# Kernel optimization log

Hardware: AMD Instinct MI355X
Metric: run time of the kernel (lower is better)

The kernel has to match this reference:

```python
import jax, jax.numpy as jnp
import numpy as np

H = 12          # num attention heads
D_HEAD = 64     # head size (768 / 12)
P = 2           # power-law exponent
C = 5.0         # score shift
EPS = 1e-10


def setup_inputs() -> dict:
    key = jax.random.key(0)
    ks = jax.random.split(key, 8)
    B, S, Dm = 32, 512, 768
    scale = 1.0 / np.sqrt(Dm)
    return {
        "hidden_states": jax.random.normal(ks[0], (B, S, Dm), dtype=jnp.float32),
        "attention_mask": jnp.ones((B, 1, 1, S), dtype=jnp.float32),
        "Wq": jax.random.normal(ks[1], (Dm, Dm), dtype=jnp.float32) * scale,
        "bq": jnp.zeros((Dm,), dtype=jnp.float32),
        "Wk": jax.random.normal(ks[2], (Dm, Dm), dtype=jnp.float32) * scale,
        "bk": jnp.zeros((Dm,), dtype=jnp.float32),
        "Wv": jax.random.normal(ks[3], (Dm, Dm), dtype=jnp.float32) * scale,
        "bv": jnp.zeros((Dm,), dtype=jnp.float32),
    }


def _heads(x, B, S):
    # [B, S, H*d] -> [B, H, S, d]
    return x.reshape(B, S, H, D_HEAD).transpose(0, 2, 1, 3)


def reference(hidden_states, attention_mask, Wq, bq, Wk, bk, Wv, bv):
    B, S, Dm = hidden_states.shape
    q = _heads(hidden_states @ Wq + bq, B, S)
    k = _heads(hidden_states @ Wk + bk, B, S)
    v = _heads(hidden_states @ Wv + bv, B, S)

    inv_sqrt_d = 1.0 / (np.sqrt(D_HEAD) + 1e-10)
    scores = jnp.einsum("bhqd,bhkd->bhqk", q, k) * inv_sqrt_d  # [B,H,S,S]

    # Power-law attention (Powerformer, distill=0 branch)
    probs = jnp.power(scores + C, P)
    probs = probs / (jnp.sum(probs, axis=-1, keepdims=True) + EPS)
    probs = probs * attention_mask  # mask multiplied after normalization

    ctx = jnp.einsum("bhqk,bhkd->bhqd", probs, v)  # [B,H,S,d]
    ctx = ctx.transpose(0, 2, 1, 3).reshape(B, S, Dm)
    return ctx
```

## Files before the change

### kernel.cpp

```cpp
#include <hip/hip_runtime.h>

typedef __attribute__((ext_vector_type(8))) _Float16 half8;
typedef __attribute__((ext_vector_type(4))) _Float16 half4;
typedef __attribute__((ext_vector_type(4))) float f32x4;

#define MFMA16(a, b, c) __builtin_amdgcn_mfma_f32_16x16x32_f16((a), (b), (c), 0, 0, 0)


__global__ __launch_bounds__(256) void wcast_kernel(
    const float* __restrict__ W0, const float* __restrict__ W1,
    const float* __restrict__ W2,
    _Float16* __restrict__ T0, _Float16* __restrict__ T1,
    _Float16* __restrict__ T2)
{
    int z = blockIdx.z;
    const float* W = (z == 0) ? W0 : (z == 1) ? W1 : W2;
    _Float16* T = (z == 0) ? T0 : (z == 1) ? T1 : T2;
    __shared__ float tile[32][33];
    int n0 = blockIdx.x * 32, k0 = blockIdx.y * 32;
    int tx = threadIdx.x & 31, ty = threadIdx.x >> 5;
#pragma unroll
    for (int r = 0; r < 4; ++r)
        tile[ty + 8 * r][tx] = W[(size_t)(k0 + ty + 8 * r) * 768 + n0 + tx];
    __syncthreads();
#pragma unroll
    for (int r = 0; r < 4; ++r)
        T[(size_t)(n0 + ty + 8 * r) * 768 + k0 + tx] =
            (_Float16)tile[tx][ty + 8 * r];
}

__global__ __launch_bounds__(256) void qkv_gemm(
    const float* __restrict__ X,
    const _Float16* __restrict__ W0, const _Float16* __restrict__ W1,
    const _Float16* __restrict__ W2,
    const float* __restrict__ b0, const float* __restrict__ b1,
    const float* __restrict__ b2,
    _Float16* __restrict__ Qo, _Float16* __restrict__ Ko,
    _Float16* __restrict__ Vo)
{
    int z = blockIdx.z;
    const _Float16* Wt = (z == 0) ? W0 : (z == 1) ? W1 : W2;
    const float* bias = (z == 0) ? b0 : (z == 1) ? b1 : b2;
    _Float16* outp = (z == 0) ? Qo : (z == 1) ? Ko : Vo;

    int m0 = blockIdx.x * 128;
    int n0 = blockIdx.y * 128;

    __shared__ _Float16 As[128 * 40];
    __shared__ _Float16 Bs[128 * 40];

    int t = threadIdx.x;
    int wave = t >> 6, lane = t & 63, quad = lane >> 4, l16 = lane & 15;
    int wm = (wave & 1) * 64, wn = (wave >> 1) * 64;
    int arow = t >> 1, ahalf = t & 1;

    f32x4 acc[4][4] = {};

    for (int k0 = 0; k0 < 768; k0 += 32) {
        {
            const float* xp = X + (size_t)(m0 + arow) * 768 + k0 + ahalf * 16;
            float4 x0 = ((const float4*)xp)[0];
            float4 x1 = ((const float4*)xp)[1];
            float4 x2 = ((const float4*)xp)[2];
            float4 x3 = ((const float4*)xp)[3];
            half8 h0, h1;
            h0[0] = (_Float16)x0.x; h0[1] = (_Float16)x0.y;
            h0[2] = (_Float16)x0.z; h0[3] = (_Float16)x0.w;
            h0[4] = (_Float16)x1.x; h0[5] = (_Float16)x1.y;
            h0[6] = (_Float16)x1.z; h0[7] = (_Float16)x1.w;
            h1[0] = (_Float16)x2.x; h1[1] = (_Float16)x2.y;
            h1[2] = (_Float16)x2.z; h1[3] = (_Float16)x2.w;
            h1[4] = (_Float16)x3.x; h1[5] = (_Float16)x3.y;
            h1[6] = (_Float16)x3.z; h1[7] = (_Float16)x3.w;
            *(half8*)&As[arow * 40 + ahalf * 16] = h0;
            *(half8*)&As[arow * 40 + ahalf * 16 + 8] = h1;
        }
        {
            const _Float16* wp = Wt + (size_t)(n0 + arow) * 768 + k0 + ahalf * 16;
            half8 w0v = ((const half8*)wp)[0];
            half8 w1v = ((const half8*)wp)[1];
            *(half8*)&Bs[arow * 40 + ahalf * 16] = w0v;
            *(half8*)&Bs[arow * 40 + ahalf * 16 + 8] = w1v;
        }
        __syncthreads();

        half8 af[4], bfr[4];
#pragma unroll
        for (int i = 0; i < 4; ++i)
            af[i] = *(const half8*)&As[(wm + i * 16 + l16) * 40 + quad * 8];
#pragma unroll
        for (int j = 0; j < 4; ++j)
            bfr[j] = *(const half8*)&Bs[(wn + j * 16 + l16) * 40 + quad * 8];
#pragma unroll
        for (int i = 0; i < 4; ++i)
#pragma unroll
            for (int j = 0; j < 4; ++j)
                acc[i][j] = MFMA16(af[i], bfr[j], acc[i][j]);
        __syncthreads();
    }

#pragma unroll
    for (int j = 0; j < 4; ++j) {
        int n = n0 + wn + j * 16 + l16;
        float bv = bias[n];
        int hh = n >> 6, d = n & 63;
#pragma unroll
        for (int i = 0; i < 4; ++i) {
            int mbase = m0 + wm + i * 16 + quad * 4;
            if (z < 2) {
#pragma unroll
                for (int r = 0; r < 4; ++r) {
                    int m = mbase + r;
                    int bb = m >> 9, s = m & 511;
                    size_t off = (((size_t)(bb * 12 + hh)) * 512 + s) * 64 + d;
                    outp[off] = (_Float16)(acc[i][j][r] + bv);
                }
            } else {
                int bb = mbase >> 9, s = mbase & 511;
                half4 pk;
#pragma unroll
                for (int r = 0; r < 4; ++r)
                    pk[r] = (_Float16)(acc[i][j][r] + bv);
                size_t off = (((size_t)(bb * 12 + hh)) * 64 + d) * 512 + s;
                *(half4*)&outp[off] = pk;
            }
        }
    }
}

__global__ __launch_bounds__(256) void attn_kernel(
    const _Float16* __restrict__ Q, const _Float16* __restrict__ K,
    const _Float16* __restrict__ Vt, const float* __restrict__ mask,
    float* __restrict__ out)
{
    __shared__ _Float16 Ks[64 * 72];
    __shared__ _Float16 Vs[64 * 72];
    __shared__ _Float16 Ps[4][32 * 72];
    __shared__ float Ms[64];

    int t = threadIdx.x;
    int wave = t >> 6, lane = t & 63, quad = lane >> 4, l16 = lane & 15;
    int qt = blockIdx.x, h = blockIdx.y, b = blockIdx.z;
    size_t bh = (size_t)b * 12 + h;
    const _Float16* Qp = Q + bh * (512 * 64);
    const _Float16* Kp = K + bh * (512 * 64);
    const _Float16* Vp = Vt + bh * (64 * 512);
    int qbase = qt * 128 + wave * 32;

    half8 qf[2][2];
#pragma unroll
    for (int i = 0; i < 2; ++i)
#pragma unroll
        for (int ks = 0; ks < 2; ++ks)
            qf[i][ks] = *(const half8*)(Qp + (size_t)(qbase + i * 16 + l16) * 64 +
                                        ks * 32 + quad * 8);

    f32x4 ctx[2][4] = {};
    float rs[2][4] = {};

    int skey = t >> 2, spart = t & 3;

    for (int kt = 0; kt < 8; ++kt) {
        int k0 = kt * 64;
        __syncthreads();
        {
            const half8* kg = (const half8*)(Kp + (size_t)(k0 + skey) * 64 + spart * 16);
            half8 a0 = kg[0], a1 = kg[1];
            *(half8*)&Ks[skey * 72 + spart * 16] = a0;
            *(half8*)&Ks[skey * 72 + spart * 16 + 8] = a1;
            const half8* vg = (const half8*)(Vp + (size_t)skey * 512 + k0 + spart * 16);
            half8 v0 = vg[0], v1 = vg[1];
            *(half8*)&Vs[skey * 72 + spart * 16] = v0;
            *(half8*)&Vs[skey * 72 + spart * 16 + 8] = v1;
            if (t < 64) Ms[t] = mask[(size_t)b * 512 + k0 + t];
        }
        __syncthreads();

#pragma unroll
        for (int i = 0; i < 2; ++i) {
#pragma unroll
            for (int n = 0; n < 4; ++n) {
                f32x4 sc = {0.f, 0.f, 0.f, 0.f};
#pragma unroll
                for (int ks = 0; ks < 2; ++ks) {
                    half8 kf = *(const half8*)&Ks[(n * 16 + l16) * 72 + ks * 32 + quad * 8];
                    sc = MFMA16(qf[i][ks], kf, sc);
                }
                float mk = Ms[n * 16 + l16];
#pragma unroll
                for (int r = 0; r < 4; ++r) {
                    float s = sc[r] * 0.125f + 5.0f;
                    float w = s * s;
                    rs[i][r] += w;
                    Ps[wave][(i * 16 + quad * 4 + r) * 72 + n * 16 + l16] =
                        (_Float16)(w * mk);
                }
            }
        }
        __syncthreads();

#pragma unroll
        for (int i = 0; i < 2; ++i) {
#pragma unroll
            for (int ks = 0; ks < 2; ++ks) {
                half8 pf = *(const half8*)&Ps[wave][(i * 16 + l16) * 72 + ks * 32 + quad * 8];
#pragma unroll
                for (int n = 0; n < 4; ++n) {
                    half8 vf = *(const half8*)&Vs[(n * 16 + l16) * 72 + ks * 32 + quad * 8];
                    ctx[i][n] = MFMA16(pf, vf, ctx[i][n]);
                }
            }
        }
    }

#pragma unroll
    for (int i = 0; i < 2; ++i)
#pragma unroll
        for (int r = 0; r < 4; ++r) {
            float v = rs[i][r];
            v += __shfl_xor(v, 1, 64);
            v += __shfl_xor(v, 2, 64);
            v += __shfl_xor(v, 4, 64);
            v += __shfl_xor(v, 8, 64);
            rs[i][r] = 1.0f / (v + 1e-10f);
        }
#pragma unroll
    for (int i = 0; i < 2; ++i)
#pragma unroll
        for (int n = 0; n < 4; ++n)
#pragma unroll
            for (int r = 0; r < 4; ++r) {
                int q = qbase + i * 16 + quad * 4 + r;
                int d = n * 16 + l16;
                out[((size_t)b * 512 + q) * 768 + h * 64 + d] =
                    ctx[i][n][r] * rs[i][r];
            }
}

extern "C" void kernel_launch(void* const* d_in, const int* in_sizes, int n_in,
                              void* d_out, int out_size, void* d_ws, size_t ws_size,
                              hipStream_t stream)
{
    const float* hs   = (const float*)d_in[0];
    const float* mask = (const float*)d_in[1];
    const float* Wq   = (const float*)d_in[2];
    const float* bq   = (const float*)d_in[3];
    const float* Wk   = (const float*)d_in[4];
    const float* bk   = (const float*)d_in[5];
    const float* Wv   = (const float*)d_in[6];
    const float* bv   = (const float*)d_in[7];
    float* out = (float*)d_out;

    char* ws = (char*)d_ws;
    _Float16* Wtq = (_Float16*)ws;
    _Float16* Wtk = Wtq + 768 * 768;
    _Float16* Wtv = Wtk + 768 * 768;
    _Float16* Qb  = Wtv + 768 * 768;
    _Float16* Kb  = Qb + 16384 * 768;
    _Float16* Vb  = Kb + 16384 * 768;

    wcast_kernel<<<dim3(24, 24, 3), 256, 0, stream>>>(Wq, Wk, Wv, Wtq, Wtk, Wtv);
    qkv_gemm<<<dim3(128, 6, 3), 256, 0, stream>>>(hs, Wtq, Wtk, Wtv,
                                                  bq, bk, bv, Qb, Kb, Vb);
    attn_kernel<<<dim3(4, 12, 32), 256, 0, stream>>>(Qb, Kb, Vb, mask, out);
}
```

Baseline: 266.0 us.

## Pre-cast X, async LDS loads in QKV GEMM, register-resident P in attention

Adds a separate kernel that casts X to fp16, staging it in the output buffer. The QKV GEMM now loads tiles with global_load_lds into XOR-swizzled unpadded LDS instead of converting in the loop. The key mask is folded into V at projection time. Attention now keeps the power-law probabilities in registers as MFMA operands, computing scores transposed and using 16x16x16 MFMAs with a ones vector for the row sums. This drops the P round-trip through LDS and one barrier per tile, and each 128-thread block gives its waves 64 queries. The GEMM loop is still single-buffered, and the extra cast kernel adds a full pass over X in global memory.

```diff
diff --git a/kernel.cpp b/kernel.cpp
--- a/kernel.cpp
+++ b/kernel.cpp
@@ -4,8 +4,29 @@
 typedef __attribute__((ext_vector_type(4))) _Float16 half4;
 typedef __attribute__((ext_vector_type(4))) float f32x4;
 
-#define MFMA16(a, b, c) __builtin_amdgcn_mfma_f32_16x16x32_f16((a), (b), (c), 0, 0, 0)
-
+#define MFMA_K32(a, b, c) __builtin_amdgcn_mfma_f32_16x16x32_f16((a), (b), (c), 0, 0, 0)
+#define MFMA_K16(a, b, c) __builtin_amdgcn_mfma_f32_16x16x16f16((a), (b), (c), 0, 0, 0)
+
+__device__ inline void async16(const _Float16* g, _Float16* l) {
+    __builtin_amdgcn_global_load_lds(
+        (const __attribute__((address_space(1))) void*)g,
+        (__attribute__((address_space(3))) void*)l, 16, 0, 0);
+}
+
+
+__global__ __launch_bounds__(256) void xcast(const float* __restrict__ X,
+                                             _Float16* __restrict__ Xh)
+{
+    size_t idx = ((size_t)blockIdx.x * 256 + threadIdx.x) * 8;
+    float4 a = *(const float4*)(X + idx);
+    float4 c = *(const float4*)(X + idx + 4);
+    half8 hv;
+    hv[0] = (_Float16)a.x; hv[1] = (_Float16)a.y;
+    hv[2] = (_Float16)a.z; hv[3] = (_Float16)a.w;
+    hv[4] = (_Float16)c.x; hv[5] = (_Float16)c.y;
+    hv[6] = (_Float16)c.z; hv[7] = (_Float16)c.w;
+    *(half8*)(Xh + idx) = hv;
+}
 
 __global__ __launch_bounds__(256) void wcast_kernel(
     const float* __restrict__ W0, const float* __restrict__ W1,
@@ -30,75 +51,75 @@
 }
 
 __global__ __launch_bounds__(256) void qkv_gemm(
-    const float* __restrict__ X,
+    const _Float16* __restrict__ Xh,
     const _Float16* __restrict__ W0, const _Float16* __restrict__ W1,
     const _Float16* __restrict__ W2,
     const float* __restrict__ b0, const float* __restrict__ b1,
     const float* __restrict__ b2,
+    const float* __restrict__ mask,
     _Float16* __restrict__ Qo, _Float16* __restrict__ Ko,
     _Float16* __restrict__ Vo)
 {
-    int z = blockIdx.z;
+    int z = blockIdx.y / 6;
+    int n0 = (blockIdx.y % 6) * 128;
+    int m0 = blockIdx.x * 128;
     const _Float16* Wt = (z == 0) ? W0 : (z == 1) ? W1 : W2;
     const float* bias = (z == 0) ? b0 : (z == 1) ? b1 : b2;
-    _Float16* outp = (z == 0) ? Qo : (z == 1) ? Ko : Vo;
-
-    int m0 = blockIdx.x * 128;
-    int n0 = blockIdx.y * 128;
-
-    __shared__ _Float16 As[128 * 40];
-    __shared__ _Float16 Bs[128 * 40];
+
+    __shared__ __attribute__((aligned(16))) _Float16 As[128 * 32];
+    __shared__ __attribute__((aligned(16))) _Float16 Bs[128 * 32];
 
     int t = threadIdx.x;
     int wave = t >> 6, lane = t & 63, quad = lane >> 4, l16 = lane & 15;
     int wm = (wave & 1) * 64, wn = (wave >> 1) * 64;
-    int arow = t >> 1, ahalf = t & 1;
+
+    int srow0 = t >> 2;
+    int sblk = (t & 3) ^ ((srow0 >> 1) & 3);
+
+    const _Float16* ga0 = Xh + (size_t)(m0 + srow0) * 768 + sblk * 8;
+    const _Float16* ga1 = Xh + (size_t)(m0 + 64 + srow0) * 768 + sblk * 8;
+    const _Float16* gb0 = Wt + (size_t)(n0 + srow0) * 768 + sblk * 8;
+    const _Float16* gb1 = Wt + (size_t)(n0 + 64 + srow0) * 768 + sblk * 8;
+    _Float16* la0 = As + wave * 512;
+    _Float16* la1 = As + 2048 + wave * 512;
+    _Float16* lb0 = Bs + wave * 512;
+    _Float16* lb1 = Bs + 2048 + wave * 512;
+
+    int swz = ((quad ^ ((l16 >> 1) & 3)) << 3);
 
     f32x4 acc[4][4] = {};
 
     for (int k0 = 0; k0 < 768; k0 += 32) {
-        {
-            const float* xp = X + (size_t)(m0 + arow) * 768 + k0 + ahalf * 16;
-            float4 x0 = ((const float4*)xp)[0];
-            float4 x1 = ((const float4*)xp)[1];
-            float4 x2 = ((const float4*)xp)[2];
-            float4 x3 = ((const float4*)xp)[3];
-            half8 h0, h1;
-            h0[0] = (_Float16)x0.x; h0[1] = (_Float16)x0.y;
-            h0[2] = (_Float16)x0.z; h0[3] = (_Float16)x0.w;
-            h0[4] = (_Float16)x1.x; h0[5] = (_Float16)x1.y;
-            h0[6] = (_Float16)x1.z; h0[7] = (_Float16)x1.w;
-            h1[0] = (_Float16)x2.x; h1[1] = (_Float16)x2.y;
-            h1[2] = (_Float16)x2.z; h1[3] = (_Float16)x2.w;
-            h1[4] = (_Float16)x3.x; h1[5] = (_Float16)x3.y;
-            h1[6] = (_Float16)x3.z; h1[7] = (_Float16)x3.w;
-            *(half8*)&As[arow * 40 + ahalf * 16] = h0;
-            *(half8*)&As[arow * 40 + ahalf * 16 + 8] = h1;
+        async16(ga0, la0); async16(ga1, la1);
+        async16(gb0, lb0); async16(gb1, lb1);
+        ga0 += 32; ga1 += 32; gb0 += 32; gb1 += 32;
+        __syncthreads();
+        half8 af[4], bf[4];
+#pragma unroll
+        for (int i = 0; i < 4; ++i)
+            af[i] = *(const half8*)&As[(wm + i * 16 + l16) * 32 + swz];
+#pragma unroll
+        for (int j = 0; j < 4; ++j)
+            bf[j] = *(const half8*)&Bs[(wn + j * 16 + l16) * 32 + swz];
+#pragma unroll
+        for (int i = 0; i < 4; ++i)
+#pragma unroll
+            for (int j = 0; j < 4; ++j)
+                acc[i][j] = MFMA_K32(af[i], bf[j], acc[i][j]);
+        __syncthreads();
+    }
+
+    float mk[4][4];
+    if (z == 2) {
+#pragma unroll
+        for (int i = 0; i < 4; ++i) {
+            int mbase = m0 + wm + i * 16 + quad * 4;
+            int bb = mbase >> 9, s = mbase & 511;
+#pragma unroll
+            for (int r = 0; r < 4; ++r)
+                mk[i][r] = mask[(size_t)bb * 512 + s + r];
         }
-        {
-            const _Float16* wp = Wt + (size_t)(n0 + arow) * 768 + k0 + ahalf * 16;
-            half8 w0v = ((const half8*)wp)[0];
-            half8 w1v = ((const half8*)wp)[1];
-            *(half8*)&Bs[arow * 40 + ahalf * 16] = w0v;
-            *(half8*)&Bs[arow * 40 + ahalf * 16 + 8] = w1v;
-        }
-        __syncthreads();
-
-        half8 af[4], bfr[4];
-#pragma unroll
-        for (int i = 0; i < 4; ++i)
-            af[i] = *(const half8*)&As[(wm + i * 16 + l16) * 40 + quad * 8];
-#pragma unroll
-        for (int j = 0; j < 4; ++j)
-            bfr[j] = *(const half8*)&Bs[(wn + j * 16 + l16) * 40 + quad * 8];
-#pragma unroll
-        for (int i = 0; i < 4; ++i)
-#pragma unroll
-            for (int j = 0; j < 4; ++j)
-                acc[i][j] = MFMA16(af[i], bfr[j], acc[i][j]);
-        __syncthreads();
-    }
-
+    }
 #pragma unroll
     for (int j = 0; j < 4; ++j) {
         int n = n0 + wn + j * 16 + l16;
@@ -107,125 +128,114 @@
 #pragma unroll
         for (int i = 0; i < 4; ++i) {
             int mbase = m0 + wm + i * 16 + quad * 4;
+            int bb = mbase >> 9, s = mbase & 511;
             if (z < 2) {
+                _Float16* outp = (z == 0) ? Qo : Ko;
 #pragma unroll
                 for (int r = 0; r < 4; ++r) {
-                    int m = mbase + r;
-                    int bb = m >> 9, s = m & 511;
-                    size_t off = (((size_t)(bb * 12 + hh)) * 512 + s) * 64 + d;
+                    size_t off = (((size_t)(bb * 12 + hh)) * 512 + s + r) * 64 + d;
                     outp[off] = (_Float16)(acc[i][j][r] + bv);
                 }
             } else {
-                int bb = mbase >> 9, s = mbase & 511;
                 half4 pk;
 #pragma unroll
                 for (int r = 0; r < 4; ++r)
-                    pk[r] = (_Float16)(acc[i][j][r] + bv);
+                    pk[r] = (_Float16)((acc[i][j][r] + bv) * mk[i][r]);
                 size_t off = (((size_t)(bb * 12 + hh)) * 64 + d) * 512 + s;
-                *(half4*)&outp[off] = pk;
+                *(half4*)&Vo[off] = pk;
             }
         }
     }
 }
 
-__global__ __launch_bounds__(256) void attn_kernel(
+__global__ __launch_bounds__(128) void attn_kernel(
     const _Float16* __restrict__ Q, const _Float16* __restrict__ K,
-    const _Float16* __restrict__ Vt, const float* __restrict__ mask,
-    float* __restrict__ out)
-{
-    __shared__ _Float16 Ks[64 * 72];
-    __shared__ _Float16 Vs[64 * 72];
-    __shared__ _Float16 Ps[4][32 * 72];
-    __shared__ float Ms[64];
+    const _Float16* __restrict__ Vt, float* __restrict__ out)
+{
+    __shared__ __attribute__((aligned(16))) _Float16 Ks[64 * 88];
+    __shared__ __attribute__((aligned(16))) _Float16 Vs[64 * 88];
 
     int t = threadIdx.x;
     int wave = t >> 6, lane = t & 63, quad = lane >> 4, l16 = lane & 15;
-    int qt = blockIdx.x, h = blockIdx.y, b = blockIdx.z;
+    int h = blockIdx.y, b = blockIdx.z;
     size_t bh = (size_t)b * 12 + h;
     const _Float16* Qp = Q + bh * (512 * 64);
     const _Float16* Kp = K + bh * (512 * 64);
     const _Float16* Vp = Vt + bh * (64 * 512);
-    int qbase = qt * 128 + wave * 32;
-
-    half8 qf[2][2];
-#pragma unroll
-    for (int i = 0; i < 2; ++i)
+    int qbase = blockIdx.x * 128 + wave * 64;
+
+    half8 qf[4][2];
+#pragma unroll
+    for (int i = 0; i < 4; ++i)
 #pragma unroll
         for (int ks = 0; ks < 2; ++ks)
             qf[i][ks] = *(const half8*)(Qp + (size_t)(qbase + i * 16 + l16) * 64 +
                                         ks * 32 + quad * 8);
 
-    f32x4 ctx[2][4] = {};
-    float rs[2][4] = {};
-
-    int skey = t >> 2, spart = t & 3;
+    f32x4 ctx[4][4] = {};
+    f32x4 rsum[4] = {};
+    const half4 ones = {(_Float16)1.f, (_Float16)1.f, (_Float16)1.f, (_Float16)1.f};
+
+    int srow = t >> 1, spart = (t & 1) * 32;
 
     for (int kt = 0; kt < 8; ++kt) {
         int k0 = kt * 64;
-        __syncthreads();
-        {
-            const half8* kg = (const half8*)(Kp + (size_t)(k0 + skey) * 64 + spart * 16);
-            half8 a0 = kg[0], a1 = kg[1];
-            *(half8*)&Ks[skey * 72 + spart * 16] = a0;
-            *(half8*)&Ks[skey * 72 + spart * 16 + 8] = a1;
-            const half8* vg = (const half8*)(Vp + (size_t)skey * 512 + k0 + spart * 16);
-            half8 v0 = vg[0], v1 = vg[1];
-            *(half8*)&Vs[skey * 72 + spart * 16] = v0;
-            *(half8*)&Vs[skey * 72 + spart * 16 + 8] = v1;
-            if (t < 64) Ms[t] = mask[(size_t)b * 512 + k0 + t];
-        }
-        __syncthreads();
-
-#pragma unroll
-        for (int i = 0; i < 2; ++i) {
-#pragma unroll
-            for (int n = 0; n < 4; ++n) {
+        const _Float16* kg = Kp + (size_t)(k0 + srow) * 64 + spart;
+        half8 ka0 = *(const half8*)kg;
+        half8 ka1 = *(const half8*)(kg + 8);
+        half8 ka2 = *(const half8*)(kg + 16);
+        half8 ka3 = *(const half8*)(kg + 24);
+        const _Float16* vg = Vp + (size_t)srow * 512 + k0 + spart;
+        half8 va0 = *(const half8*)vg;
+        half8 va1 = *(const half8*)(vg + 8);
+        half8 va2 = *(const half8*)(vg + 16);
+        half8 va3 = *(const half8*)(vg + 24);
+        __syncthreads();
+        *(half8*)&Ks[srow * 88 + spart] = ka0;
+        *(half8*)&Ks[srow * 88 + spart + 8] = ka1;
+        *(half8*)&Ks[srow * 88 + spart + 16] = ka2;
+        *(half8*)&Ks[srow * 88 + spart + 24] = ka3;
+        *(half8*)&Vs[srow * 88 + spart] = va0;
+        *(half8*)&Vs[srow * 88 + spart + 8] = va1;
+        *(half8*)&Vs[srow * 88 + spart + 16] = va2;
+        *(half8*)&Vs[srow * 88 + spart + 24] = va3;
+        __syncthreads();
+
+#pragma unroll
+        for (int kb = 0; kb < 4; ++kb) {
+            half8 kf0 = *(const half8*)&Ks[(kb * 16 + l16) * 88 + quad * 8];
+            half8 kf1 = *(const half8*)&Ks[(kb * 16 + l16) * 88 + 32 + quad * 8];
+            half4 pA[4];
+#pragma unroll
+            for (int i = 0; i < 4; ++i) {
                 f32x4 sc = {0.f, 0.f, 0.f, 0.f};
-#pragma unroll
-                for (int ks = 0; ks < 2; ++ks) {
-                    half8 kf = *(const half8*)&Ks[(n * 16 + l16) * 72 + ks * 32 + quad * 8];
-                    sc = MFMA16(qf[i][ks], kf, sc);
-                }
-                float mk = Ms[n * 16 + l16];
+                sc = MFMA_K32(kf0, qf[i][0], sc);
+                sc = MFMA_K32(kf1, qf[i][1], sc);
+                half4 p;
 #pragma unroll
                 for (int r = 0; r < 4; ++r) {
                     float s = sc[r] * 0.125f + 5.0f;
-                    float w = s * s;
-                    rs[i][r] += w;
-                    Ps[wave][(i * 16 + quad * 4 + r) * 72 + n * 16 + l16] =
-                        (_Float16)(w * mk);
+                    p[r] = (_Float16)(s * s);
                 }
+                pA[i] = p;
+                rsum[i] = MFMA_K16(p, ones, rsum[i]);
+            }
+#pragma unroll
+            for (int n = 0; n < 4; ++n) {
+                half4 vf = *(const half4*)&Vs[(n * 16 + l16) * 88 + kb * 16 + quad * 4];
+#pragma unroll
+                for (int i = 0; i < 4; ++i)
+                    ctx[i][n] = MFMA_K16(pA[i], vf, ctx[i][n]);
             }
         }
-        __syncthreads();
-
-#pragma unroll
-        for (int i = 0; i < 2; ++i) {
-#pragma unroll
-            for (int ks = 0; ks < 2; ++ks) {
-                half8 pf = *(const half8*)&Ps[wave][(i * 16 + l16) * 72 + ks * 32 + quad * 8];
-#pragma unroll
-                for (int n = 0; n < 4; ++n) {
-                    half8 vf = *(const half8*)&Vs[(n * 16 + l16) * 72 + ks * 32 + quad * 8];
-                    ctx[i][n] = MFMA16(pf, vf, ctx[i][n]);
-                }
-            }
-        }
-    }
-
-#pragma unroll
-    for (int i = 0; i < 2; ++i)
-#pragma unroll
-        for (int r = 0; r < 4; ++r) {
-            float v = rs[i][r];
-            v += __shfl_xor(v, 1, 64);
-            v += __shfl_xor(v, 2, 64);
-            v += __shfl_xor(v, 4, 64);
-            v += __shfl_xor(v, 8, 64);
-            rs[i][r] = 1.0f / (v + 1e-10f);
-        }
-#pragma unroll
-    for (int i = 0; i < 2; ++i)
+    }
+
+#pragma unroll
+    for (int i = 0; i < 4; ++i) {
+        f32x4 inv;
+#pragma unroll
+        for (int r = 0; r < 4; ++r)
+            inv[r] = 1.0f / (rsum[i][r] + 1e-10f);
 #pragma unroll
         for (int n = 0; n < 4; ++n)
 #pragma unroll
@@ -233,8 +243,9 @@
                 int q = qbase + i * 16 + quad * 4 + r;
                 int d = n * 16 + l16;
                 out[((size_t)b * 512 + q) * 768 + h * 64 + d] =
-                    ctx[i][n][r] * rs[i][r];
-            }
+                    ctx[i][n][r] * inv[r];
+            }
+    }
 }
 
 extern "C" void kernel_launch(void* const* d_in, const int* in_sizes, int n_in,
@@ -258,9 +269,11 @@
     _Float16* Qb  = Wtv + 768 * 768;
     _Float16* Kb  = Qb + 16384 * 768;
     _Float16* Vb  = Kb + 16384 * 768;
-
+    _Float16* Xh = (_Float16*)d_out;
+
+    xcast<<<dim3(6144), 256, 0, stream>>>(hs, Xh);
     wcast_kernel<<<dim3(24, 24, 3), 256, 0, stream>>>(Wq, Wk, Wv, Wtq, Wtk, Wtv);
-    qkv_gemm<<<dim3(128, 6, 3), 256, 0, stream>>>(hs, Wtq, Wtk, Wtv,
-                                                  bq, bk, bv, Qb, Kb, Vb);
-    attn_kernel<<<dim3(4, 12, 32), 256, 0, stream>>>(Qb, Kb, Vb, mask, out);
-}
+    qkv_gemm<<<dim3(128, 18), 256, 0, stream>>>(Xh, Wtq, Wtk, Wtv,
+                                                bq, bk, bv, mask, Qb, Kb, Vb);
+    attn_kernel<<<dim3(4, 12, 32), 128, 0, stream>>>(Qb, Kb, Vb, out);
+}
```

Result: no change. 267.1 us (+0.4%).
